# Kernel tuning notes

Hardware: AMD Instinct MI355X
Metric: run time of the kernel (lower is better)

The kernel has to match this reference:

```python
import jax, jax.numpy as jnp
import numpy as np

EMBED_DIM = 1024
NUM_HEADS = 16
D_K = EMBED_DIM // NUM_HEADS


def setup_inputs() -> dict:
    key = jax.random.key(0)
    ks = jax.random.split(key, 5)
    x = jax.random.normal(ks[0], (2, 2048, EMBED_DIM), dtype=jnp.float32)
    # kaiming_normal on 2D params: std = sqrt(2/fan_in) with fan_in = in_features
    w_qkv = jax.random.normal(ks[1], (3 * EMBED_DIM, EMBED_DIM), dtype=jnp.float32) * np.sqrt(2.0 / EMBED_DIM)
    b_qkv = jnp.zeros((3 * EMBED_DIM,), dtype=jnp.float32)
    w_o = jax.random.normal(ks[2], (EMBED_DIM, EMBED_DIM), dtype=jnp.float32) * np.sqrt(2.0 / EMBED_DIM)
    b_o = jnp.zeros((EMBED_DIM,), dtype=jnp.float32)
    return {"x": x, "w_qkv": w_qkv, "b_qkv": b_qkv, "w_o": w_o, "b_o": b_o}


def reference(x, w_qkv, b_qkv, w_o, b_o):
    B, N, C = x.shape
    qkv = x @ w_qkv.T + b_qkv  # [B,N,3C]
    q, k, v = jnp.split(qkv, 3, axis=-1)
    # [B,H,N,d_k]
    q = q.reshape(B, N, NUM_HEADS, D_K).transpose(0, 2, 1, 3)
    k = k.reshape(B, N, NUM_HEADS, D_K).transpose(0, 2, 1, 3)
    v = v.reshape(B, N, NUM_HEADS, D_K).transpose(0, 2, 1, 3)
    # NOTE: original forward scales by 1/sqrt(embed_dim), not 1/sqrt(d_k)
    scores = jnp.einsum('bhqd,bhkd->bhqk', q, k) / np.sqrt(C).astype(np.float32)
    causal = jnp.tril(jnp.ones((N, N), dtype=bool))
    scores = jnp.where(causal, scores, -jnp.inf)
    attn = jax.nn.softmax(scores, axis=-1)
    out = jnp.einsum('bhqk,bhkd->bhqd', attn, v)  # [B,H,N,d_k]
    out = out.transpose(0, 2, 1, 3).reshape(B, N, C)
    return out @ w_o.T + b_o
```

## Files before the change

kernel.cpp:

```cpp
#include <hip/hip_runtime.h>
#include <hip/hip_bf16.h>
#include <math.h>

typedef __bf16 bf16_t;
typedef __bf16 bf16x8 __attribute__((ext_vector_type(8)));
typedef __bf16 bf16x4 __attribute__((ext_vector_type(4)));
typedef __bf16 bf16x2 __attribute__((ext_vector_type(2)));
typedef float f32x4 __attribute__((ext_vector_type(4)));
typedef unsigned u32x4 __attribute__((ext_vector_type(4)));

#define SCALE_L2E 0.045084234f
#define ROUND_B 0.0028169f

#define MFMA16(a, b, c) __builtin_amdgcn_mfma_f32_16x16x32_bf16(a, b, c, 0, 0, 0)

__device__ __forceinline__ unsigned pack2(float a, float b) {
  return __builtin_amdgcn_perm(__builtin_bit_cast(unsigned, b),
                               __builtin_bit_cast(unsigned, a), 0x07060302u);
}

__global__ void convert3_f32_bf16(const float* __restrict__ a, int na,
                                  const float* __restrict__ b, int nb,
                                  const float* __restrict__ c, int nc,
                                  bf16_t* __restrict__ oa, bf16_t* __restrict__ ob,
                                  bf16_t* __restrict__ oc) {
  int i = (blockIdx.x * blockDim.x + threadIdx.x) * 8;
  const float* src;
  bf16_t* dst;
  int off;
  if (i < na) { src = a; dst = oa; off = i; }
  else if (i < na + nb) { src = b; dst = ob; off = i - na; }
  else if (i < na + nb + nc) { src = c; dst = oc; off = i - na - nb; }
  else return;
  float4 u = *(const float4*)&src[off];
  float4 v = *(const float4*)&src[off + 4];
  bf16x8 w = {(bf16_t)u.x, (bf16_t)u.y, (bf16_t)u.z, (bf16_t)u.w,
              (bf16_t)v.x, (bf16_t)v.y, (bf16_t)v.z, (bf16_t)v.w};
  *(bf16x8*)&dst[off] = w;
}

#define GLOBAL_AS __attribute__((address_space(1)))
#define LDS_AS __attribute__((address_space(3)))
__device__ __forceinline__ void g2l16(const void* g, void* l) {
  __builtin_amdgcn_global_load_lds((const GLOBAL_AS void*)g, (LDS_AS void*)l,
                                   16, 0, 0);
}

template <int BM, typename TC>
__launch_bounds__(256, 2)
__global__ void gemm128db(const bf16_t* __restrict__ A,
                          const bf16_t* __restrict__ B,
                          const float* __restrict__ bias,
                          TC* __restrict__ C,
                          int M, int N, int K) {
  constexpr int MF = BM / 32;
  __shared__ __align__(16) bf16_t Ab[2][BM * 64];
  __shared__ __align__(16) bf16_t Bb[2][128 * 64];

  const int tid = threadIdx.x;
  const int wave = tid >> 6, lane = tid & 63, quad = lane >> 4, ln = lane & 15;
  const int wm = wave >> 1, wn = wave & 1;
  const int m0 = blockIdx.y * BM, n0 = blockIdx.x * 128;
  const int nt = K >> 6;

  const int rowoff = wave * 8 + (lane >> 3);
  const int c8 = ((lane & 7) ^ (lane >> 3)) * 8;
  const int w8row = wave * 8;
  const bf16_t* Arow0 = A + (size_t)(m0 + rowoff) * K + c8;
  const bf16_t* Brow0 = B + (size_t)(n0 + rowoff) * K + c8;

  auto stA = [&](int tl) {
    const bf16_t* g = Arow0 + (size_t)tl * 64;
    bf16_t* l = &Ab[tl & 1][w8row * 64];
#pragma unroll
    for (int rr = 0; rr < BM; rr += 32)
      g2l16(g + (size_t)rr * K, l + rr * 64);
  };
  auto stB = [&](int tl) {
    const bf16_t* g = Brow0 + (size_t)tl * 64;
    bf16_t* l = &Bb[tl & 1][w8row * 64];
#pragma unroll
    for (int rr = 0; rr < 128; rr += 32)
      g2l16(g + (size_t)rr * K, l + rr * 64);
  };

  const int cswl = (quad ^ (ln & 7)) * 8;
  const int aBase = (wm * (BM / 2) + ln) * 64;
  const int bBase = (wn * 64 + ln) * 64;

  f32x4 acc[MF][4];
#pragma unroll
  for (int i = 0; i < MF; i++)
#pragma unroll
    for (int j = 0; j < 4; j++) acc[i][j] = (f32x4){0.f, 0.f, 0.f, 0.f};

  bf16x8 af[MF][2], bfr[4][2];

  auto ldA = [&](int buf) {
#pragma unroll
    for (int mf = 0; mf < MF; ++mf)
#pragma unroll
      for (int sk = 0; sk < 2; ++sk)
        af[mf][sk] = *(const bf16x8*)&Ab[buf][aBase + mf * 1024 +
                                             (cswl ^ (sk << 5))];
  };
  auto ldB = [&](int buf) {
#pragma unroll
    for (int nf = 0; nf < 4; ++nf)
#pragma unroll
      for (int sk = 0; sk < 2; ++sk)
        bfr[nf][sk] = *(const bf16x8*)&Bb[buf][bBase + nf * 1024 +
                                               (cswl ^ (sk << 5))];
  };
  auto mm = [&]() {
#pragma unroll
    for (int mf = 0; mf < MF; ++mf)
#pragma unroll
      for (int nf = 0; nf < 4; ++nf) {
        f32x4 c = acc[mf][nf];
        c = MFMA16(af[mf][0], bfr[nf][0], c);
        c = MFMA16(af[mf][1], bfr[nf][1], c);
        acc[mf][nf] = c;
      }
  };

  stA(0); stB(0);
  __syncthreads();

  for (int tl = 0; tl < nt; ++tl) {
    const int buf = tl & 1;
    if (tl + 1 < nt) { stA(tl + 1); stB(tl + 1); }
    ldA(buf);
    ldB(buf);
    mm();
    __syncthreads();
  }

#pragma unroll
  for (int nf = 0; nf < 4; ++nf) {
    const int col = n0 + wn * 64 + nf * 16 + ln;
    const float bv = bias[col];
#pragma unroll
    for (int mf = 0; mf < MF; ++mf) {
      const int row = m0 + wm * (BM / 2) + mf * 16 + quad * 4;
#pragma unroll
      for (int r = 0; r < 4; ++r)
        C[(size_t)(row + r) * N + col] = (TC)(acc[mf][nf][r] + bv);
    }
  }
}

__launch_bounds__(512, 4)
__global__ void attn_kernel(const bf16_t* __restrict__ qkv,
                            bf16_t* __restrict__ out) {
  constexpr int KP = 72, VP = 72;
  constexpr int BUF = 64 * KP;
  __shared__ __align__(16) bf16_t KsB[2 * BUF];
  __shared__ __align__(16) bf16_t VtB[2 * BUF];

  const int t = threadIdx.x;
  const int wave = t >> 6, lane = t & 63, quad = lane >> 4, ln = lane & 15;
  const int qw = wave & 3;
  const int kh = wave >> 2;
  const int p = blockIdx.x >> 5;
  const int bh = blockIdx.x & 31;
  const int b = bh >> 4, h = bh & 15;
  const int qA = p * 64, qB = (31 - p) * 64;
  const int ntiles = 32 - p;
  const size_t rs = 3072;
  const size_t base = (size_t)b * 2048 * rs;

  const size_t qoffA = base + (size_t)(qA + qw * 16 + ln) * rs + h * 64;
  const size_t qoffB = base + (size_t)(qB + qw * 16 + ln) * rs + h * 64;
  bf16x8 qfA0 = *(const bf16x8*)&qkv[qoffA + quad * 8];
  bf16x8 qfA1 = *(const bf16x8*)&qkv[qoffA + 32 + quad * 8];
  bf16x8 qfB0 = *(const bf16x8*)&qkv[qoffB + quad * 8];
  bf16x8 qfB1 = *(const bf16x8*)&qkv[qoffB + 32 + quad * 8];

  f32x4 oA[4], oB[4];
  f32x4 lAv = (f32x4){0.f, 0.f, 0.f, 0.f};
  f32x4 lBv = (f32x4){0.f, 0.f, 0.f, 0.f};
  for (int ct = 0; ct < 4; ct++) {
    oA[ct] = (f32x4){0.f, 0.f, 0.f, 0.f};
    oB[ct] = (f32x4){0.f, 0.f, 0.f, 0.f};
  }

  const int t256 = t & 255;
  const int r0 = t256 >> 3, c0 = (t256 & 7) * 8;
  const int wav4 = t256 >> 6;
  const int ksA = r0 * KP + (((t256 & 7) + wav4) & 7) * 8;
  const int ksB2 = (r0 + 32) * KP + (((t256 & 7) + wav4 + 4) & 7) * 8;
  const int vkoff = ((((r0 >> 2) + (t256 & 7)) & 7)) * 8 + 2 * (r0 & 3);

  const bf16_t* gp0;
  const bf16_t* gp1;
  if (kh) {
    gp0 = &qkv[base + 1024 + h * 64 + (size_t)r0 * rs + c0];
    gp1 = gp0 + (size_t)32 * rs;
  } else {
    gp0 = &qkv[base + 2048 + h * 64 + (size_t)(2 * r0) * rs + c0];
    gp1 = gp0 + rs;
  }
  const size_t tstep = (size_t)64 * rs;

  bf16x8 s0 = *(const bf16x8*)gp0; gp0 += tstep;
  bf16x8 s1 = *(const bf16x8*)gp1; gp1 += tstep;

  const int qgA = qA + qw * 16 + ln;
  const int qgB = qB + qw * 16 + ln;

  auto stage_to = [&](int buf) {
    if (kh) {
      bf16_t* KsW = &KsB[buf * BUF];
      *(bf16x8*)&KsW[ksA] = s0;
      *(bf16x8*)&KsW[ksB2] = s1;
    } else {
      bf16_t* VtW = &VtB[buf * BUF];
#pragma unroll
      for (int j = 0; j < 8; j++) {
        bf16x2 w2 = {s0[j], s1[j]};
        *(bf16x2*)&VtW[(c0 + j) * VP + vkoff] = w2;
      }
    }
  };
  auto prefetch = [&]() {
    s0 = *(const bf16x8*)gp0; gp0 += tstep;
    s1 = *(const bf16x8*)gp1; gp1 += tstep;
  };
  auto load_kfs = [&](const bf16_t* Ks, bf16x8* kf0s, bf16x8* kf1s) {
#pragma unroll
    for (int sh = 0; sh < 2; sh++) {
      const int st = kh * 2 + sh;
      const int krow = st * 16 + ln;
      const int rot = 2 * st + (ln >> 3);
      kf0s[sh] = *(const bf16x8*)&Ks[krow * KP + ((quad + rot) & 7) * 8];
      kf1s[sh] = *(const bf16x8*)&Ks[krow * KP + ((quad + 4 + rot) & 7) * 8];
    }
  };
  auto qk_block = [&](const bf16x8* kf0s, const bf16x8* kf1s, bf16x8 q0,
                      bf16x8 q1, f32x4& lxv, bf16x8& Bp, bool masked,
                      int kbase, int qg) {
    u32x4 u;
#pragma unroll
    for (int sh = 0; sh < 2; sh++) {
      f32x4 s = (f32x4){0.f, 0.f, 0.f, 0.f};
      __builtin_amdgcn_s_setprio(1);
      s = MFMA16(kf0s[sh], q0, s);
      s = MFMA16(kf1s[sh], q1, s);
      __builtin_amdgcn_s_setprio(0);
      const int k0g = kbase + (kh * 2 + sh) * 16 + quad * 4;
      float pv[4];
#pragma unroll
      for (int r = 0; r < 4; r++) {
        float e = __builtin_amdgcn_exp2f(fmaf(s[r], SCALE_L2E, ROUND_B));
        if (masked && (k0g + r > qg)) e = 0.f;
        lxv[r] += e;
        pv[r] = e;
      }
      u[sh * 2] = pack2(pv[0], pv[1]);
      u[sh * 2 + 1] = pack2(pv[2], pv[3]);
    }
    Bp = __builtin_bit_cast(bf16x8, u);
  };
  auto load_vfs = [&](const bf16_t* Vt, bf16x8* A8s) {
#pragma unroll
    for (int ct = 0; ct < 4; ct++) {
      const int dd = ct * 16 + ln;
      const int bc = (quad >> 1) + 2 * ct + (ln >> 3);
      const int cA = (4 * kh + bc) & 7;
      const int cB = (4 * kh + 2 + bc) & 7;
      bf16x4 v0 = *(const bf16x4*)&Vt[dd * VP + cA * 8 + (quad & 1) * 4];
      bf16x4 v1 = *(const bf16x4*)&Vt[dd * VP + cB * 8 + (quad & 1) * 4];
      A8s[ct] = __builtin_shufflevector(v0, v1, 0, 1, 2, 3, 4, 5, 6, 7);
    }
  };

  auto body = [&](int kt, bool hasA, bool maskA, bool maskB) {
    if (kt + 1 < ntiles) {
      stage_to((kt + 1) & 1);
      if (kt + 2 < ntiles) prefetch();
    }
    const bf16_t* Ks = &KsB[(kt & 1) * BUF];
    const bf16_t* Vt = &VtB[(kt & 1) * BUF];
    bf16x8 kf0s[2], kf1s[2];
    load_kfs(Ks, kf0s, kf1s);
    bf16x8 BpA, BpB;
    if (hasA) qk_block(kf0s, kf1s, qfA0, qfA1, lAv, BpA, maskA, kt * 64, qgA);
    qk_block(kf0s, kf1s, qfB0, qfB1, lBv, BpB, maskB, kt * 64, qgB);
    bf16x8 A8s[4];
    load_vfs(Vt, A8s);
    __builtin_amdgcn_s_setprio(1);
#pragma unroll
    for (int ct = 0; ct < 4; ct++) {
      if (hasA) oA[ct] = MFMA16(A8s[ct], BpA, oA[ct]);
      oB[ct] = MFMA16(A8s[ct], BpB, oB[ct]);
    }
    __builtin_amdgcn_s_setprio(0);
    if (kt + 1 < ntiles) __syncthreads();
  };

  stage_to(0);
  if (ntiles > 1) prefetch();
  __syncthreads();

  for (int kt = 0; kt < p; kt++) body(kt, true, false, false);
  body(p, true, true, false);
  for (int kt = p + 1; kt < 31 - p; kt++) body(kt, false, false, false);
  body(31 - p, false, false, true);

  float lAx = (lAv[0] + lAv[1]) + (lAv[2] + lAv[3]);
  float lBx = (lBv[0] + lBv[1]) + (lBv[2] + lBv[3]);
  lAx += __shfl_xor(lAx, 16);
  lAx += __shfl_xor(lAx, 32);
  lBx += __shfl_xor(lBx, 16);
  lBx += __shfl_xor(lBx, 32);

  __syncthreads();
  float* redA = (float*)KsB;
  float* redB = (float*)VtB;
  const int idx = qw * 64 + lane;
  if (kh) {
#pragma unroll
    for (int ct = 0; ct < 4; ct++) {
      *(f32x4*)&redA[(ct * 256 + idx) * 4] = oA[ct];
      *(f32x4*)&redB[(ct * 256 + idx) * 4] = oB[ct];
    }
    redA[4096 + idx] = lAx;
    redB[4096 + idx] = lBx;
  }
  __syncthreads();
  if (!kh) {
#pragma unroll
    for (int ct = 0; ct < 4; ct++) {
      oA[ct] += *(const f32x4*)&redA[(ct * 256 + idx) * 4];
      oB[ct] += *(const f32x4*)&redB[(ct * 256 + idx) * 4];
    }
    lAx += redA[4096 + idx];
    lBx += redB[4096 + idx];
    const float invA = __builtin_amdgcn_rcpf(lAx);
    const float invB = __builtin_amdgcn_rcpf(lBx);
    const int ocol = h * 64 + quad * 4;
#pragma unroll
    for (int ct = 0; ct < 4; ct++) {
      bf16x4 wa, wb;
#pragma unroll
      for (int r = 0; r < 4; r++) {
        wa[r] = (bf16_t)(oA[ct][r] * invA);
        wb[r] = (bf16_t)(oB[ct][r] * invB);
      }
      *(bf16x4*)&out[(size_t)(b * 2048 + qgA) * 1024 + ocol + ct * 16] = wa;
      *(bf16x4*)&out[(size_t)(b * 2048 + qgB) * 1024 + ocol + ct * 16] = wb;
    }
  }
}

extern "C" void kernel_launch(void* const* d_in, const int* in_sizes, int n_in,
                              void* d_out, int out_size, void* d_ws, size_t ws_size,
                              hipStream_t stream) {
  const float* x     = (const float*)d_in[0];
  const float* w_qkv = (const float*)d_in[1];
  const float* b_qkv = (const float*)d_in[2];
  const float* w_o   = (const float*)d_in[3];
  const float* b_o   = (const float*)d_in[4];
  float* out = (float*)d_out;

  bf16_t* qkv   = (bf16_t*)d_ws;
  bf16_t* xbf   = qkv + (size_t)4096 * 3072;
  bf16_t* wqkvb = xbf + (size_t)4096 * 1024;
  bf16_t* wob   = wqkvb + (size_t)3072 * 1024;
  bf16_t* attn  = xbf;

  const int na = 4096 * 1024, nb = 3072 * 1024, nc = 1024 * 1024;
  convert3_f32_bf16<<<dim3((na + nb + nc) / (256 * 8)), 256, 0, stream>>>(
      x, na, w_qkv, nb, w_o, nc, xbf, wqkvb, wob);

  gemm128db<128, bf16_t><<<dim3(3072 / 128, 4096 / 128), 256, 0, stream>>>(
      xbf, wqkvb, b_qkv, qkv, 4096, 3072, 1024);
  attn_kernel<<<dim3(512), 512, 0, stream>>>(qkv, attn);
  gemm128db<64, float><<<dim3(1024 / 128, 4096 / 64), 256, 0, stream>>>(
      attn, wob, b_o, out, 4096, 1024, 1024);
}
```

Baseline: 172.8 us.

## Add K=32 double-buffered QKV GEMM kernel with higher occupancy

Replaces the QKV projection GEMM with a new kernel that uses a K-tile of 32 instead of 64. This halves LDS per block and allows four blocks per CU through launch bounds. Tiles are loaded with XOR-swizzled direct global-to-LDS loads and double buffering, and each wave computes a 64x64 tile with 16x16x32 MFMAs. The cost is twice as many K iterations and barriers, each with less MFMA work to cover load latency.

New measurement: 167.9 us, median of 2. 1.03x faster.

```diff
diff --git a/kernel.cpp b/kernel.cpp
--- a/kernel.cpp
+++ b/kernel.cpp
@@ -46,6 +46,80 @@
                                    16, 0, 0);
 }
 
+__launch_bounds__(256, 4)
+__global__ void gemm128k32(const bf16_t* __restrict__ A,
+                           const bf16_t* __restrict__ B,
+                           const float* __restrict__ bias,
+                           bf16_t* __restrict__ C,
+                           int M, int N, int K) {
+  __shared__ __align__(16) bf16_t As[2][128 * 32];
+  __shared__ __align__(16) bf16_t Bs[2][128 * 32];
+
+  const int t = threadIdx.x;
+  const int wave = t >> 6, lane = t & 63, quad = lane >> 4, ln = lane & 15;
+  const int wm = (wave >> 1) * 64, wn = (wave & 1) * 64;
+  const int m0 = blockIdx.y * 128, n0 = blockIdx.x * 128;
+  const int nt = K >> 5;
+
+  const int srow = lane >> 2;
+  const int schunk = ((lane & 3) ^ ((lane >> 3) & 3)) * 8;
+  const bf16_t* gA0 = &A[(size_t)(m0 + wave * 32 + srow) * K + schunk];
+  const bf16_t* gA1 = gA0 + (size_t)16 * K;
+  const bf16_t* gB0 = &B[(size_t)(n0 + wave * 32 + srow) * K + schunk];
+  const bf16_t* gB1 = gB0 + (size_t)16 * K;
+
+  const int cslot = (quad ^ ((ln >> 1) & 3)) * 8;
+
+  f32x4 acc[4][4];
+#pragma unroll
+  for (int i = 0; i < 4; i++)
+#pragma unroll
+    for (int j = 0; j < 4; j++) acc[i][j] = (f32x4){0.f, 0.f, 0.f, 0.f};
+
+  auto stage = [&](int tl) {
+    const int buf = tl & 1;
+    const int k0 = tl * 32;
+    g2l16(gA0 + k0, &As[buf][(wave * 32) * 32]);
+    g2l16(gA1 + k0, &As[buf][(wave * 32 + 16) * 32]);
+    g2l16(gB0 + k0, &Bs[buf][(wave * 32) * 32]);
+    g2l16(gB1 + k0, &Bs[buf][(wave * 32 + 16) * 32]);
+  };
+
+  stage(0);
+  __syncthreads();
+
+  for (int tl = 0; tl < nt; ++tl) {
+    const int buf = tl & 1;
+    if (tl + 1 < nt) stage(tl + 1);
+    bf16x8 af[4], bfr[4];
+#pragma unroll
+    for (int mt = 0; mt < 4; mt++)
+      af[mt] = *(const bf16x8*)&As[buf][(wm + mt * 16 + ln) * 32 + cslot];
+#pragma unroll
+    for (int nf = 0; nf < 4; nf++)
+      bfr[nf] = *(const bf16x8*)&Bs[buf][(wn + nf * 16 + ln) * 32 + cslot];
+#pragma unroll
+    for (int mt = 0; mt < 4; mt++)
+#pragma unroll
+      for (int nf = 0; nf < 4; nf++)
+        acc[mt][nf] = MFMA16(af[mt], bfr[nf], acc[mt][nf]);
+    __syncthreads();
+  }
+
+#pragma unroll
+  for (int nf = 0; nf < 4; nf++) {
+    const int col = n0 + wn + nf * 16 + ln;
+    const float bv = bias[col];
+#pragma unroll
+    for (int mt = 0; mt < 4; mt++) {
+      const int row = m0 + wm + mt * 16 + quad * 4;
+#pragma unroll
+      for (int r = 0; r < 4; r++)
+        C[(size_t)(row + r) * N + col] = (bf16_t)(acc[mt][nf][r] + bv);
+    }
+  }
+}
+
 template <int BM, typename TC>
 __launch_bounds__(256, 2)
 __global__ void gemm128db(const bf16_t* __restrict__ A,
@@ -374,7 +448,7 @@
   convert3_f32_bf16<<<dim3((na + nb + nc) / (256 * 8)), 256, 0, stream>>>(
       x, na, w_qkv, nb, w_o, nc, xbf, wqkvb, wob);
 
-  gemm128db<128, bf16_t><<<dim3(3072 / 128, 4096 / 128), 256, 0, stream>>>(
+  gemm128k32<<<dim3(3072 / 128, 4096 / 128), 256, 0, stream>>>(
       xbf, wqkvb, b_qkv, qkv, 4096, 3072, 1024);
   attn_kernel<<<dim3(512), 512, 0, stream>>>(qkv, attn);
   gemm128db<64, float><<<dim3(1024 / 128, 4096 / 64), 256, 0, stream>>>(
```
